# Optimization experiments

Hardware: AMD Instinct MI355X
Metric: run time of the kernel (lower is better)

The kernel has to match this reference:

```python
import jax, jax.numpy as jnp
import numpy as np

B = 1024          # batch
H = 1024          # rnn_num_hidden
T = 512           # max_length (encoder timesteps)
NUM = 44          # numeric features
EMB = [(30490, 64), (7, 8), (12, 8), (3, 4)]
IN = NUM + sum(d for _, d in EMB)   # input_size = 128


def lstm_cell(x, h, c, w_ih, w_hh, b_ih, b_hh):
    # PyTorch LSTM gate order: i, f, g, o
    g = x @ w_ih.T + h @ w_hh.T + b_ih + b_hh
    i, f, gg, o = jnp.split(g, 4, axis=-1)
    c2 = jax.nn.sigmoid(f) * c + jax.nn.sigmoid(i) * jnp.tanh(gg)
    h2 = jax.nn.sigmoid(o) * jnp.tanh(c2)
    return h2, c2


def setup_inputs():
    key = jax.random.key(0)
    ks = iter(jax.random.split(key, 32))
    nrm = lambda shape, s=0.02: (s * jax.random.normal(next(ks), shape)).astype(jnp.float32)
    return {
        "x": nrm((B, 1, NUM), 1.0),
        "x_emb": jax.random.randint(next(ks), (B, 1, 4), 0, 3),
        "h0": nrm((2, B, H), 1.0),
        "c0": nrm((2, B, H), 1.0),
        "encoder_outputs": nrm((T, B, H), 1.0),
        "emb0": nrm(EMB[0]), "emb1": nrm(EMB[1]), "emb2": nrm(EMB[2]), "emb3": nrm(EMB[3]),
        "attn_w": nrm((T, IN + 2 * H)), "attn_b": nrm((T,)),
        "comb_w": nrm((IN, IN + H)), "comb_b": nrm((IN,)),
        "w_ih0": nrm((4 * H, IN)), "w_hh0": nrm((4 * H, H)),
        "b_ih0": nrm((4 * H,)), "b_hh0": nrm((4 * H,)),
        "w_ih1": nrm((4 * H, H)), "w_hh1": nrm((4 * H, H)),
        "b_ih1": nrm((4 * H,)), "b_hh1": nrm((4 * H,)),
        "pred_w": nrm((1, H)), "pred_b": nrm((1,)),
    }


def reference(x, x_emb, h0, c0, encoder_outputs, emb0, emb1, emb2, emb3,
              attn_w, attn_b, comb_w, comb_b,
              w_ih0, w_hh0, b_ih0, b_hh0, w_ih1, w_hh1, b_ih1, b_hh1,
              pred_w, pred_b):
    xt = x.transpose(1, 0, 2)[0]                       # (B, NUM)
    ids = x_emb.transpose(1, 0, 2)[0]                  # (B, 4)
    e = jnp.concatenate([emb0[ids[:, 0]], emb1[ids[:, 1]],
                         emb2[ids[:, 2]], emb3[ids[:, 3]]], axis=1)
    x_rnn = jnp.concatenate([xt, e], axis=1)           # (B, IN)
    attn_in = jnp.concatenate([x_rnn, h0[0], c0[0]], axis=1)       # (B, IN+2H)
    aw = jax.nn.softmax(attn_in @ attn_w.T + attn_b, axis=1)       # (B, T)
    ctx = jnp.einsum('bt,tbh->bh', aw, encoder_outputs)            # (B, H)
    comb = jnp.concatenate([x_rnn, ctx], axis=1) @ comb_w.T + comb_b  # (B, IN)
    h1, c1 = lstm_cell(comb, h0[0], c0[0], w_ih0, w_hh0, b_ih0, b_hh0)
    h2, c2 = lstm_cell(h1, h0[1], c0[1], w_ih1, w_hh1, b_ih1, b_hh1)
    out = h2 @ pred_w.T + pred_b                       # (B, 1)
    return out, (jnp.stack([h1, h2]), jnp.stack([c1, c2])), aw
```

## Files before the change

kernel.cpp:

```cpp
#include <hip/hip_runtime.h>
#include <hip/hip_bf16.h>

#define B 1024
#define H 1024
#define T 512
#define NUM 44
#define IN 128
#define AK (IN + 2 * H)
#define XC (IN + H)
#define G4 (4 * H)
#define BH ((size_t)B * H)

typedef __attribute__((ext_vector_type(8))) short s16x8;
typedef __attribute__((ext_vector_type(4))) float f32x4;

__device__ __forceinline__ unsigned short f2bf(float f) {
    unsigned u = __float_as_uint(f);
    unsigned r = (u + 0x7fffu + ((u >> 16) & 1u)) >> 16;
    return (unsigned short)r;
}
__device__ __forceinline__ float bf2f(unsigned short u) {
    return __uint_as_float(((unsigned)u) << 16);
}
__device__ __forceinline__ float sigmf(float v) { return 1.0f / (1.0f + expf(-v)); }

__device__ __forceinline__ void gload16(const ushort* g, ushort* l) {
    __builtin_amdgcn_global_load_lds(
        (const __attribute__((address_space(1))) void*)g,
        (__attribute__((address_space(3))) void*)l,
        16, 0, 0);
}

#define TM 128
#define TN 128
#define TK 32

__device__ __forceinline__ void gemm_core(
    const ushort* __restrict__ X, const ushort* __restrict__ W,
    float* __restrict__ Cf, ushort* __restrict__ Cb,
    int kbeg, int kend, int ldx, int ldw, int ldc,
    int m0, int n0, ushort (*As)[TK], ushort (*Bs)[TK])
{
    const int tid = threadIdx.x;
    const int lane = tid & 63;
    const int wid = tid >> 6;
    const int wm = wid >> 1, wn = wid & 1;
    const int srow = wid * 32 + (lane >> 2);
    const int skc  = (lane & 3) * 8;

    f32x4 acc[4][4] = {};

    for (int k0 = kbeg; k0 < kend; k0 += TK) {
        gload16(X + (size_t)(m0 + srow) * ldx + k0 + skc,      &As[wid * 32][0]);
        gload16(X + (size_t)(m0 + srow + 16) * ldx + k0 + skc, &As[wid * 32 + 16][0]);
        gload16(W + (size_t)(n0 + srow) * ldw + k0 + skc,      &Bs[wid * 32][0]);
        gload16(W + (size_t)(n0 + srow + 16) * ldw + k0 + skc, &Bs[wid * 32 + 16][0]);
        __syncthreads();

        s16x8 a[4], b[4];
        #pragma unroll
        for (int m = 0; m < 4; ++m)
            a[m] = *(const s16x8*)&As[wm * 64 + m * 16 + (lane & 15)][(lane >> 4) * 8];
        #pragma unroll
        for (int n = 0; n < 4; ++n)
            b[n] = *(const s16x8*)&Bs[wn * 64 + n * 16 + (lane & 15)][(lane >> 4) * 8];
        #pragma unroll
        for (int m = 0; m < 4; ++m)
            #pragma unroll
            for (int n = 0; n < 4; ++n)
                acc[m][n] = __builtin_amdgcn_mfma_f32_16x16x32_bf16(a[m], b[n], acc[m][n], 0, 0, 0);
        __syncthreads();
    }

    #pragma unroll
    for (int m = 0; m < 4; ++m) {
        #pragma unroll
        for (int n = 0; n < 4; ++n) {
            int col = n0 + wn * 64 + n * 16 + (lane & 15);
            #pragma unroll
            for (int j = 0; j < 4; ++j) {
                int row = m0 + wm * 64 + m * 16 + (lane >> 4) * 4 + j;
                float v = acc[m][n][j];
                if (Cf) Cf[(size_t)row * ldc + col] = v;
                if (Cb) Cb[(size_t)row * ldc + col] = f2bf(v);
            }
        }
    }
}

__global__ __launch_bounds__(256) void allgemms_kernel(
    const ushort* __restrict__ attn_in, const ushort* __restrict__ attn_w_bf,
    float* __restrict__ logits_p,
    const ushort* __restrict__ h0_bf,
    const ushort* __restrict__ whh0_bf, const ushort* __restrict__ whh1_bf,
    ushort* __restrict__ g1part, ushort* __restrict__ g2part,
    const ushort* __restrict__ wih0_bf, const ushort* __restrict__ comb_wT_bf,
    ushort* __restrict__ W_f_bf)
{
    __shared__ ushort As[TM][TK];
    __shared__ ushort Bs[TN][TK];
    const int rid = blockIdx.x;
    if (rid < 128) {
        int z = rid >> 5, t = rid & 31;
        int m0 = (t >> 2) * TM, n0 = (t & 3) * TN;
        gemm_core(attn_in, attn_w_bf, logits_p + (size_t)z * B * T, nullptr,
                  z * 544, z * 544 + 544, AK, AK, T, m0, n0, As, Bs);
    } else if (rid < 640) {
        int layer = (rid - 128) >> 8;
        int t = (rid - 128) & 255;
        int m0 = (t >> 5) * TM, n0 = (t & 31) * TN;
        gemm_core(h0_bf + (size_t)layer * BH, layer ? whh1_bf : whh0_bf,
                  nullptr, layer ? g2part : g1part,
                  0, H, H, H, G4, m0, n0, As, Bs);
    } else {
        int t = rid - 640;
        int m0 = (t / 9) * TM, n0 = (t % 9) * TN;
        gemm_core(wih0_bf, comb_wT_bf, nullptr, W_f_bf,
                  0, IN, IN, IN, XC, m0, n0, As, Bs);
    }
}

__global__ __launch_bounds__(256) void gemm64_kernel(
    const ushort* __restrict__ X, const ushort* __restrict__ W,
    const float* __restrict__ bias1, const float* __restrict__ bias2,
    const ushort* __restrict__ CinBf, ushort* __restrict__ Cb,
    int K, int ldx, int ldw, int ldc)
{
    __shared__ ushort As[64][TK];
    __shared__ ushort Bs[128][TK];
    const int tid = threadIdx.x;
    const int lane = tid & 63;
    const int wid = tid >> 6;
    const int wm = wid >> 1, wn = wid & 1;
    const int m0 = blockIdx.y * 64;
    const int n0 = blockIdx.x * 128;
    const int skc = (lane & 3) * 8;

    f32x4 acc[2][4] = {};

    for (int k0 = 0; k0 < K; k0 += TK) {
        gload16(X + (size_t)(m0 + wid * 16 + (lane >> 2)) * ldx + k0 + skc, &As[wid * 16][0]);
        gload16(W + (size_t)(n0 + wid * 32 + (lane >> 2)) * ldw + k0 + skc, &Bs[wid * 32][0]);
        gload16(W + (size_t)(n0 + wid * 32 + 16 + (lane >> 2)) * ldw + k0 + skc, &Bs[wid * 32 + 16][0]);
        __syncthreads();
        s16x8 a[2], b[4];
        #pragma unroll
        for (int m = 0; m < 2; ++m)
            a[m] = *(const s16x8*)&As[wm * 32 + m * 16 + (lane & 15)][(lane >> 4) * 8];
        #pragma unroll
        for (int n = 0; n < 4; ++n)
            b[n] = *(const s16x8*)&Bs[wn * 64 + n * 16 + (lane & 15)][(lane >> 4) * 8];
        #pragma unroll
        for (int m = 0; m < 2; ++m)
            #pragma unroll
            for (int n = 0; n < 4; ++n)
                acc[m][n] = __builtin_amdgcn_mfma_f32_16x16x32_bf16(a[m], b[n], acc[m][n], 0, 0, 0);
        __syncthreads();
    }

    #pragma unroll
    for (int m = 0; m < 2; ++m) {
        #pragma unroll
        for (int n = 0; n < 4; ++n) {
            int col = n0 + wn * 64 + n * 16 + (lane & 15);
            float badd = (bias1 ? bias1[col] : 0.f) + (bias2 ? bias2[col] : 0.f);
            #pragma unroll
            for (int j = 0; j < 4; ++j) {
                int row = m0 + wm * 32 + m * 16 + (lane >> 4) * 4 + j;
                float v = acc[m][n][j] + badd + bf2f(CinBf[(size_t)row * ldc + col]);
                Cb[(size_t)row * ldc + col] = f2bf(v);
            }
        }
    }
}

#define P0 2048
#define P1 (P0 + 1088)
#define P2 (P1 + 512)
#define P3 (P2 + 4096)
#define P4 (P3 + 4096)
#define P5 (P4 + 4096)
#define P6 (P5 + 576)
#define P7 (P6 + 16)
#define P8 (P7 + 1024)

__global__ __launch_bounds__(256) void preamble_kernel(
    const float* __restrict__ h0, const float* __restrict__ attn_w,
    const float* __restrict__ w_ih0, const float* __restrict__ w_hh0,
    const float* __restrict__ w_ih1, const float* __restrict__ w_hh1,
    const float* __restrict__ comb_w, const float* __restrict__ comb_b,
    const float* __restrict__ b_ih0, const float* __restrict__ b_hh0,
    const float* __restrict__ x, const int* __restrict__ x_emb,
    const float* __restrict__ c0,
    const float* __restrict__ e0, const float* __restrict__ e1,
    const float* __restrict__ e2, const float* __restrict__ e3,
    ushort* __restrict__ h0_bf, ushort* __restrict__ attn_w_bf,
    ushort* __restrict__ wih0_bf, ushort* __restrict__ whh0_bf,
    ushort* __restrict__ wih1_bf, ushort* __restrict__ whh1_bf,
    ushort* __restrict__ comb_wT, float* __restrict__ biasf,
    ushort* __restrict__ attn_in, ushort* __restrict__ xctx)
{
    const int bid = blockIdx.x;
    const int tid = threadIdx.x;

    if (bid < P5) {
        const float* s; ushort* d; int f;
        if (bid < P0)      { f = bid * 256 + tid;        s = h0;     d = h0_bf; }
        else if (bid < P1) { f = (bid - P0) * 256 + tid; s = attn_w; d = attn_w_bf; }
        else if (bid < P2) { f = (bid - P1) * 256 + tid; s = w_ih0;  d = wih0_bf; }
        else if (bid < P3) { f = (bid - P2) * 256 + tid; s = w_hh0;  d = whh0_bf; }
        else if (bid < P4) { f = (bid - P3) * 256 + tid; s = w_ih1;  d = wih1_bf; }
        else               { f = (bid - P4) * 256 + tid; s = w_hh1;  d = whh1_bf; }
        float4 v = ((const float4*)s)[f];
        ushort4 o = {f2bf(v.x), f2bf(v.y), f2bf(v.z), f2bf(v.w)};
        ((ushort4*)d)[f] = o;
    } else if (bid < P6) {
        int e = (bid - P5) * 256 + tid;
        int j = e >> 7, k = e & 127;
        comb_wT[e] = f2bf(comb_w[(size_t)k * XC + j]);
    } else if (bid < P7) {
        __shared__ float cb[IN];
        for (int i = tid; i < IN; i += 256) cb[i] = comb_b[i];
        __syncthreads();
        int i = (bid - P6) * 256 + tid;
        float s = b_ih0[i] + b_hh0[i];
        const float* row = w_ih0 + (size_t)i * IN;
        #pragma unroll 8
        for (int j = 0; j < IN; ++j) s += row[j] * cb[j];
        biasf[i] = s;
    } else {
        int b = bid - P7;
        int id0 = x_emb[b * 4 + 0];
        int id1 = x_emb[b * 4 + 1];
        int id2 = x_emb[b * 4 + 2];
        int id3 = x_emb[b * 4 + 3];
        ushort* dst = attn_in + (size_t)b * AK;
        for (int j = tid; j < AK; j += 256) {
            float v;
            if (j < 44)        v = x[b * NUM + j];
            else if (j < 108)  v = e0[id0 * 64 + (j - 44)];
            else if (j < 116)  v = e1[id1 * 8 + (j - 108)];
            else if (j < 124)  v = e2[id2 * 8 + (j - 116)];
            else if (j < 128)  v = e3[id3 * 4 + (j - 124)];
            else if (j < 1152) v = h0[b * H + (j - 128)];
            else               v = c0[b * H + (j - 1152)];
            unsigned short bf = f2bf(v);
            dst[j] = bf;
            if (j < IN) xctx[(size_t)b * XC + j] = bf;
        }
    }
}

__global__ __launch_bounds__(256) void softmax_kernel(
    const float* __restrict__ logits_p, const float* __restrict__ attn_b,
    float* __restrict__ aw)
{
    int b = blockIdx.x;
    int tid = threadIdx.x;
    __shared__ float red[8];
    float v0 = attn_b[tid], v1 = attn_b[tid + 256];
    #pragma unroll
    for (int z = 0; z < 4; ++z) {
        const float* lp = logits_p + (size_t)z * B * T + (size_t)b * T;
        v0 += lp[tid];
        v1 += lp[tid + 256];
    }
    float m = fmaxf(v0, v1);
    #pragma unroll
    for (int off = 32; off > 0; off >>= 1) m = fmaxf(m, __shfl_down(m, off, 64));
    if ((tid & 63) == 0) red[tid >> 6] = m;
    __syncthreads();
    m = fmaxf(fmaxf(red[0], red[1]), fmaxf(red[2], red[3]));
    float e0 = expf(v0 - m), e1 = expf(v1 - m);
    float s = e0 + e1;
    #pragma unroll
    for (int off = 32; off > 0; off >>= 1) s += __shfl_down(s, off, 64);
    if ((tid & 63) == 0) red[4 + (tid >> 6)] = s;
    __syncthreads();
    s = red[4] + red[5] + red[6] + red[7];
    float inv = 1.0f / s;
    aw[(size_t)b * T + tid]       = e0 * inv;
    aw[(size_t)b * T + tid + 256] = e1 * inv;
}

__global__ __launch_bounds__(256) void ctx_kernel(
    const float* __restrict__ enc, const float* __restrict__ aw,
    float* __restrict__ ctxp)
{
    const int b = blockIdx.x >> 1;
    const int z = blockIdx.x & 1;
    const int tid = threadIdx.x;
    __shared__ float w[256];
    w[tid] = aw[(size_t)b * T + z * 256 + tid];
    __syncthreads();

    const float* p = enc + (size_t)(z * 256) * BH + (size_t)b * H + tid * 4;
    float4 acc = {0.f, 0.f, 0.f, 0.f};
    for (int t0 = 0; t0 < 256; t0 += 8) {
        float4 vv[8];
        #pragma unroll
        for (int u = 0; u < 8; ++u)
            vv[u] = *(const float4*)(p + (size_t)(t0 + u) * BH);
        #pragma unroll
        for (int u = 0; u < 8; ++u) {
            float sw = w[t0 + u];
            acc.x += sw * vv[u].x; acc.y += sw * vv[u].y;
            acc.z += sw * vv[u].z; acc.w += sw * vv[u].w;
        }
    }
    *(float4*)(ctxp + (size_t)z * BH + (size_t)b * H + tid * 4) = acc;
}

__global__ __launch_bounds__(256) void ctx_reduce_kernel(
    const float* __restrict__ ctxp, ushort* __restrict__ xctx)
{
    int i = blockIdx.x * 256 + threadIdx.x;
    float4 a = ((const float4*)ctxp)[i];
    float4 c = ((const float4*)(ctxp + BH))[i];
    int f = i * 4;
    int b = f >> 10, h = f & 1023;
    ushort4 o = {f2bf(a.x + c.x), f2bf(a.y + c.y), f2bf(a.z + c.z), f2bf(a.w + c.w)};
    *(ushort4*)(xctx + (size_t)b * XC + IN + h) = o;
}

__global__ __launch_bounds__(256) void lstm_pointwise_kernel(
    const ushort* __restrict__ g, const float* __restrict__ c_in,
    float* __restrict__ h_out, float* __restrict__ c_out,
    ushort* __restrict__ h_bf)
{
    int q = blockIdx.x * 256 + threadIdx.x;
    int b = q >> 8;
    int j = (q & 255) * 4;
    const ushort* gr = g + (size_t)b * G4 + j;
    ushort4 gi4 = *(const ushort4*)(gr);
    ushort4 gf4 = *(const ushort4*)(gr + H);
    ushort4 gc4 = *(const ushort4*)(gr + 2 * H);
    ushort4 go4 = *(const ushort4*)(gr + 3 * H);
    size_t base = (size_t)b * H + j;
    float4 cin = *(const float4*)(c_in + base);
    float4 cv, hv;
    {
        float c0v = sigmf(bf2f(gf4.x)) * cin.x + sigmf(bf2f(gi4.x)) * tanhf(bf2f(gc4.x));
        float c1v = sigmf(bf2f(gf4.y)) * cin.y + sigmf(bf2f(gi4.y)) * tanhf(bf2f(gc4.y));
        float c2v = sigmf(bf2f(gf4.z)) * cin.z + sigmf(bf2f(gi4.z)) * tanhf(bf2f(gc4.z));
        float c3v = sigmf(bf2f(gf4.w)) * cin.w + sigmf(bf2f(gi4.w)) * tanhf(bf2f(gc4.w));
        cv = make_float4(c0v, c1v, c2v, c3v);
        hv = make_float4(sigmf(bf2f(go4.x)) * tanhf(c0v), sigmf(bf2f(go4.y)) * tanhf(c1v),
                         sigmf(bf2f(go4.z)) * tanhf(c2v), sigmf(bf2f(go4.w)) * tanhf(c3v));
    }
    *(float4*)(c_out + base) = cv;
    *(float4*)(h_out + base) = hv;
    if (h_bf) {
        ushort4 o = {f2bf(hv.x), f2bf(hv.y), f2bf(hv.z), f2bf(hv.w)};
        *(ushort4*)(h_bf + base) = o;
    }
}

__global__ __launch_bounds__(256) void pred_kernel(
    const float* __restrict__ h2, const float* __restrict__ pw,
    const float* __restrict__ pb, float* __restrict__ out)
{
    int b = blockIdx.x;
    const float* row = h2 + (size_t)b * H;
    float s = 0.f;
    for (int j = threadIdx.x; j < H; j += 256) s += row[j] * pw[j];
    #pragma unroll
    for (int off = 32; off > 0; off >>= 1) s += __shfl_down(s, off, 64);
    __shared__ float sm[4];
    if ((threadIdx.x & 63) == 0) sm[threadIdx.x >> 6] = s;
    __syncthreads();
    if (threadIdx.x == 0) out[b] = sm[0] + sm[1] + sm[2] + sm[3] + pb[0];
}

extern "C" void kernel_launch(void* const* d_in, const int* in_sizes, int n_in,
                              void* d_out, int out_size, void* d_ws, size_t ws_size,
                              hipStream_t stream) {
    (void)in_sizes; (void)n_in; (void)out_size; (void)ws_size;
    const float* x      = (const float*)d_in[0];
    const int*   x_emb  = (const int*)d_in[1];
    const float* h0     = (const float*)d_in[2];
    const float* c0     = (const float*)d_in[3];
    const float* enc    = (const float*)d_in[4];
    const float* emb0   = (const float*)d_in[5];
    const float* emb1   = (const float*)d_in[6];
    const float* emb2   = (const float*)d_in[7];
    const float* emb3   = (const float*)d_in[8];
    const float* attn_w = (const float*)d_in[9];
    const float* attn_b = (const float*)d_in[10];
    const float* comb_w = (const float*)d_in[11];
    const float* comb_b = (const float*)d_in[12];
    const float* w_ih0  = (const float*)d_in[13];
    const float* w_hh0  = (const float*)d_in[14];
    const float* b_ih0  = (const float*)d_in[15];
    const float* b_hh0  = (const float*)d_in[16];
    const float* w_ih1  = (const float*)d_in[17];
    const float* w_hh1  = (const float*)d_in[18];
    const float* b_ih1  = (const float*)d_in[19];
    const float* b_hh1  = (const float*)d_in[20];
    const float* pred_w = (const float*)d_in[21];
    const float* pred_b = (const float*)d_in[22];

    float* out = (float*)d_out;
    float* h1_out = out + 1024;
    float* h2_out = out + 1024 + BH;
    float* c1_out = out + 1024 + 2 * BH;
    float* c2_out = out + 1024 + 3 * BH;
    float* aw_out = out + 1024 + 4 * BH;

    char* w = (char*)d_ws;
    ushort* attn_in_bf = (ushort*)w;  w += (size_t)B * AK * 2;
    ushort* h0_bf      = (ushort*)w;  w += (size_t)2 * BH * 2;
    ushort* attn_w_bf  = (ushort*)w;  w += (size_t)T * AK * 2;
    ushort* wih0_bf    = (ushort*)w;  w += (size_t)G4 * IN * 2;
    ushort* whh0_bf    = (ushort*)w;  w += (size_t)G4 * H * 2;
    ushort* wih1_bf    = (ushort*)w;  w += (size_t)G4 * H * 2;
    ushort* whh1_bf    = (ushort*)w;  w += (size_t)G4 * H * 2;
    ushort* comb_wT_bf = (ushort*)w;  w += (size_t)XC * IN * 2;
    ushort* W_f_bf     = (ushort*)w;  w += (size_t)G4 * XC * 2;
    float*  bias_f     = (float*)w;   w += (size_t)G4 * 4;
    ushort* xctx_bf    = (ushort*)w;  w += (size_t)B * XC * 2;
    ushort* h1_bf      = (ushort*)w;  w += (size_t)BH * 2;
    ushort* g1part     = (ushort*)w;  w += (size_t)B * G4 * 2;
    ushort* g2part     = (ushort*)w;  w += (size_t)B * G4 * 2;
    float*  logits_p   = (float*)w;   w += (size_t)4 * B * T * 4;
    float*  ctxp       = (float*)w;   w += (size_t)2 * BH * 4;

    preamble_kernel<<<P8, 256, 0, stream>>>(
        h0, attn_w, w_ih0, w_hh0, w_ih1, w_hh1, comb_w, comb_b, b_ih0, b_hh0,
        x, x_emb, c0, emb0, emb1, emb2, emb3,
        h0_bf, attn_w_bf, wih0_bf, whh0_bf, wih1_bf, whh1_bf, comb_wT_bf, bias_f,
        attn_in_bf, xctx_bf);

    allgemms_kernel<<<928, 256, 0, stream>>>(
        attn_in_bf, attn_w_bf, logits_p,
        h0_bf, whh0_bf, whh1_bf, g1part, g2part,
        wih0_bf, comb_wT_bf, W_f_bf);

    softmax_kernel<<<B, 256, 0, stream>>>(logits_p, attn_b, aw_out);

    ctx_kernel<<<2048, 256, 0, stream>>>(enc, aw_out, ctxp);

    ctx_reduce_kernel<<<(int)(BH / 4 / 256), 256, 0, stream>>>(ctxp, xctx_bf);

    gemm64_kernel<<<dim3(G4 / 128, B / 64), 256, 0, stream>>>(
        xctx_bf, W_f_bf, bias_f, nullptr, g1part, g1part, XC, XC, XC, G4);

    lstm_pointwise_kernel<<<(int)(BH / 4 / 256), 256, 0, stream>>>(g1part, c0, h1_out, c1_out, h1_bf);

    gemm64_kernel<<<dim3(G4 / 128, B / 64), 256, 0, stream>>>(
        h1_bf, wih1_bf, b_ih1, b_hh1, g2part, g2part, H, H, H, G4);

    lstm_pointwise_kernel<<<(int)(BH / 4 / 256), 256, 0, stream>>>(g2part, c0 + BH, h2_out, c2_out, nullptr);

    pred_kernel<<<B, 256, 0, stream>>>(h2_out, pred_w, pred_b, out);
}
```

Measured before the change: 590.6 us.

## Interleave LSTM gate rows and fuse pointwise cell into the input GEMM epilogue

Weight rows of all LSTM matrices and the biases are permuted during preamble conversion so that the four gates of each hidden unit sit in adjacent output columns. The second-stage GEMM epilogue then gathers the i/f/g/o pre-activations with lane shuffles and computes c and h directly, which removes both standalone pointwise kernels and the bf16 round-trip of the full gate buffer. Only one lane in four writes, so epilogue stores become scattered and less coalesced, and the transcendentals are computed redundantly in all four lanes.

```diff
diff --git a/kernel.cpp b/kernel.cpp
--- a/kernel.cpp
+++ b/kernel.cpp
@@ -92,9 +92,9 @@
     const ushort* __restrict__ attn_in, const ushort* __restrict__ attn_w_bf,
     float* __restrict__ logits_p,
     const ushort* __restrict__ h0_bf,
-    const ushort* __restrict__ whh0_bf, const ushort* __restrict__ whh1_bf,
+    const ushort* __restrict__ whh0p, const ushort* __restrict__ whh1p,
     ushort* __restrict__ g1part, ushort* __restrict__ g2part,
-    const ushort* __restrict__ wih0_bf, const ushort* __restrict__ comb_wT_bf,
+    const ushort* __restrict__ wih0p, const ushort* __restrict__ comb_wT_bf,
     ushort* __restrict__ W_f_bf)
 {
     __shared__ ushort As[TM][TK];
@@ -109,22 +109,22 @@
         int layer = (rid - 128) >> 8;
         int t = (rid - 128) & 255;
         int m0 = (t >> 5) * TM, n0 = (t & 31) * TN;
-        gemm_core(h0_bf + (size_t)layer * BH, layer ? whh1_bf : whh0_bf,
+        gemm_core(h0_bf + (size_t)layer * BH, layer ? whh1p : whh0p,
                   nullptr, layer ? g2part : g1part,
                   0, H, H, H, G4, m0, n0, As, Bs);
     } else {
         int t = rid - 640;
         int m0 = (t / 9) * TM, n0 = (t % 9) * TN;
-        gemm_core(wih0_bf, comb_wT_bf, nullptr, W_f_bf,
+        gemm_core(wih0p, comb_wT_bf, nullptr, W_f_bf,
                   0, IN, IN, IN, XC, m0, n0, As, Bs);
     }
 }
 
-__global__ __launch_bounds__(256) void gemm64_kernel(
+__global__ __launch_bounds__(256) void gemm64_lstm_kernel(
     const ushort* __restrict__ X, const ushort* __restrict__ W,
-    const float* __restrict__ bias1, const float* __restrict__ bias2,
-    const ushort* __restrict__ CinBf, ushort* __restrict__ Cb,
-    int K, int ldx, int ldw, int ldc)
+    const float* __restrict__ biasp, const ushort* __restrict__ CinBf,
+    const float* __restrict__ c_in, float* __restrict__ h_out, float* __restrict__ c_out,
+    ushort* __restrict__ h_bf, int K)
 {
     __shared__ ushort As[64][TK];
     __shared__ ushort Bs[128][TK];
@@ -139,9 +139,9 @@
     f32x4 acc[2][4] = {};
 
     for (int k0 = 0; k0 < K; k0 += TK) {
-        gload16(X + (size_t)(m0 + wid * 16 + (lane >> 2)) * ldx + k0 + skc, &As[wid * 16][0]);
-        gload16(W + (size_t)(n0 + wid * 32 + (lane >> 2)) * ldw + k0 + skc, &Bs[wid * 32][0]);
-        gload16(W + (size_t)(n0 + wid * 32 + 16 + (lane >> 2)) * ldw + k0 + skc, &Bs[wid * 32 + 16][0]);
+        gload16(X + (size_t)(m0 + wid * 16 + (lane >> 2)) * K + k0 + skc, &As[wid * 16][0]);
+        gload16(W + (size_t)(n0 + wid * 32 + (lane >> 2)) * K + k0 + skc, &Bs[wid * 32][0]);
+        gload16(W + (size_t)(n0 + wid * 32 + 16 + (lane >> 2)) * K + k0 + skc, &Bs[wid * 32 + 16][0]);
         __syncthreads();
         s16x8 a[2], b[4];
         #pragma unroll
@@ -158,17 +158,33 @@
         __syncthreads();
     }
 
+    const int q = lane & 3;
     #pragma unroll
     for (int m = 0; m < 2; ++m) {
         #pragma unroll
         for (int n = 0; n < 4; ++n) {
             int col = n0 + wn * 64 + n * 16 + (lane & 15);
-            float badd = (bias1 ? bias1[col] : 0.f) + (bias2 ? bias2[col] : 0.f);
+            int u = col >> 2;
+            float badd = biasp[col];
             #pragma unroll
             for (int j = 0; j < 4; ++j) {
                 int row = m0 + wm * 32 + m * 16 + (lane >> 4) * 4 + j;
-                float v = acc[m][n][j] + badd + bf2f(CinBf[(size_t)row * ldc + col]);
-                Cb[(size_t)row * ldc + col] = f2bf(v);
+                float pre = acc[m][n][j] + badd + bf2f(CinBf[(size_t)row * G4 + col]);
+                float f1 = __shfl_xor(pre, 1, 64);
+                float f2 = __shfl_xor(pre, 2, 64);
+                float f3 = __shfl_xor(pre, 3, 64);
+                float gi = q == 0 ? pre : q == 1 ? f1 : q == 2 ? f2 : f3;
+                float gf = q == 0 ? f1 : q == 1 ? pre : q == 2 ? f3 : f2;
+                float gg = q == 0 ? f2 : q == 1 ? f3 : q == 2 ? pre : f1;
+                float go = q == 0 ? f3 : q == 1 ? f2 : q == 2 ? f1 : pre;
+                float cprev = c_in[(size_t)row * H + u];
+                float c = sigmf(gf) * cprev + sigmf(gi) * tanhf(gg);
+                float h = sigmf(go) * tanhf(c);
+                if (q == 0) {
+                    h_out[(size_t)row * H + u] = h;
+                    c_out[(size_t)row * H + u] = c;
+                    if (h_bf) h_bf[(size_t)row * H + u] = f2bf(h);
+                }
             }
         }
     }
@@ -182,7 +198,8 @@
 #define P5 (P4 + 4096)
 #define P6 (P5 + 576)
 #define P7 (P6 + 16)
-#define P8 (P7 + 1024)
+#define P8 (P7 + 16)
+#define P9 (P8 + 1024)
 
 __global__ __launch_bounds__(256) void preamble_kernel(
     const float* __restrict__ h0, const float* __restrict__ attn_w,
@@ -190,28 +207,42 @@
     const float* __restrict__ w_ih1, const float* __restrict__ w_hh1,
     const float* __restrict__ comb_w, const float* __restrict__ comb_b,
     const float* __restrict__ b_ih0, const float* __restrict__ b_hh0,
+    const float* __restrict__ b_ih1, const float* __restrict__ b_hh1,
     const float* __restrict__ x, const int* __restrict__ x_emb,
     const float* __restrict__ c0,
     const float* __restrict__ e0, const float* __restrict__ e1,
     const float* __restrict__ e2, const float* __restrict__ e3,
     ushort* __restrict__ h0_bf, ushort* __restrict__ attn_w_bf,
-    ushort* __restrict__ wih0_bf, ushort* __restrict__ whh0_bf,
-    ushort* __restrict__ wih1_bf, ushort* __restrict__ whh1_bf,
-    ushort* __restrict__ comb_wT, float* __restrict__ biasf,
+    ushort* __restrict__ wih0p, ushort* __restrict__ whh0p,
+    ushort* __restrict__ wih1p, ushort* __restrict__ whh1p,
+    ushort* __restrict__ comb_wT, float* __restrict__ biasf, float* __restrict__ bias2p,
     ushort* __restrict__ attn_in, ushort* __restrict__ xctx)
 {
     const int bid = blockIdx.x;
     const int tid = threadIdx.x;
 
-    if (bid < P5) {
+    if (bid < P1) {
         const float* s; ushort* d; int f;
-        if (bid < P0)      { f = bid * 256 + tid;        s = h0;     d = h0_bf; }
-        else if (bid < P1) { f = (bid - P0) * 256 + tid; s = attn_w; d = attn_w_bf; }
-        else if (bid < P2) { f = (bid - P1) * 256 + tid; s = w_ih0;  d = wih0_bf; }
-        else if (bid < P3) { f = (bid - P2) * 256 + tid; s = w_hh0;  d = whh0_bf; }
-        else if (bid < P4) { f = (bid - P3) * 256 + tid; s = w_ih1;  d = wih1_bf; }
-        else               { f = (bid - P4) * 256 + tid; s = w_hh1;  d = whh1_bf; }
+        if (bid < P0) { f = bid * 256 + tid;        s = h0;     d = h0_bf; }
+        else          { f = (bid - P0) * 256 + tid; s = attn_w; d = attn_w_bf; }
         float4 v = ((const float4*)s)[f];
+        ushort4 o = {f2bf(v.x), f2bf(v.y), f2bf(v.z), f2bf(v.w)};
+        ((ushort4*)d)[f] = o;
+    } else if (bid < P2) {
+        int f = (bid - P1) * 256 + tid;
+        int r = f >> 5, c = f & 31;
+        int srcrow = ((r & 3) << 10) + (r >> 2);
+        float4 v = ((const float4*)w_ih0)[srcrow * 32 + c];
+        ushort4 o = {f2bf(v.x), f2bf(v.y), f2bf(v.z), f2bf(v.w)};
+        ((ushort4*)wih0p)[f] = o;
+    } else if (bid < P5) {
+        const float* s; ushort* d; int f;
+        if (bid < P3)      { f = (bid - P2) * 256 + tid; s = w_hh0; d = whh0p; }
+        else if (bid < P4) { f = (bid - P3) * 256 + tid; s = w_ih1; d = wih1p; }
+        else               { f = (bid - P4) * 256 + tid; s = w_hh1; d = whh1p; }
+        int r = f >> 8, c = f & 255;
+        int srcrow = ((r & 3) << 10) + (r >> 2);
+        float4 v = ((const float4*)s)[srcrow * 256 + c];
         ushort4 o = {f2bf(v.x), f2bf(v.y), f2bf(v.z), f2bf(v.w)};
         ((ushort4*)d)[f] = o;
     } else if (bid < P6) {
@@ -222,14 +253,19 @@
         __shared__ float cb[IN];
         for (int i = tid; i < IN; i += 256) cb[i] = comb_b[i];
         __syncthreads();
-        int i = (bid - P6) * 256 + tid;
-        float s = b_ih0[i] + b_hh0[i];
-        const float* row = w_ih0 + (size_t)i * IN;
+        int p = (bid - P6) * 256 + tid;
+        int srow = ((p & 3) << 10) + (p >> 2);
+        float s = b_ih0[srow] + b_hh0[srow];
+        const float* row = w_ih0 + (size_t)srow * IN;
         #pragma unroll 8
         for (int j = 0; j < IN; ++j) s += row[j] * cb[j];
-        biasf[i] = s;
+        biasf[p] = s;
+    } else if (bid < P8) {
+        int p = (bid - P7) * 256 + tid;
+        int srow = ((p & 3) << 10) + (p >> 2);
+        bias2p[p] = b_ih1[srow] + b_hh1[srow];
     } else {
-        int b = bid - P7;
+        int b = bid - P8;
         int id0 = x_emb[b * 4 + 0];
         int id1 = x_emb[b * 4 + 1];
         int id2 = x_emb[b * 4 + 2];
@@ -321,39 +357,6 @@
     int b = f >> 10, h = f & 1023;
     ushort4 o = {f2bf(a.x + c.x), f2bf(a.y + c.y), f2bf(a.z + c.z), f2bf(a.w + c.w)};
     *(ushort4*)(xctx + (size_t)b * XC + IN + h) = o;
-}
-
-__global__ __launch_bounds__(256) void lstm_pointwise_kernel(
-    const ushort* __restrict__ g, const float* __restrict__ c_in,
-    float* __restrict__ h_out, float* __restrict__ c_out,
-    ushort* __restrict__ h_bf)
-{
-    int q = blockIdx.x * 256 + threadIdx.x;
-    int b = q >> 8;
-    int j = (q & 255) * 4;
-    const ushort* gr = g + (size_t)b * G4 + j;
-    ushort4 gi4 = *(const ushort4*)(gr);
-    ushort4 gf4 = *(const ushort4*)(gr + H);
-    ushort4 gc4 = *(const ushort4*)(gr + 2 * H);
-    ushort4 go4 = *(const ushort4*)(gr + 3 * H);
-    size_t base = (size_t)b * H + j;
-    float4 cin = *(const float4*)(c_in + base);
-    float4 cv, hv;
-    {
-        float c0v = sigmf(bf2f(gf4.x)) * cin.x + sigmf(bf2f(gi4.x)) * tanhf(bf2f(gc4.x));
-        float c1v = sigmf(bf2f(gf4.y)) * cin.y + sigmf(bf2f(gi4.y)) * tanhf(bf2f(gc4.y));
-        float c2v = sigmf(bf2f(gf4.z)) * cin.z + sigmf(bf2f(gi4.z)) * tanhf(bf2f(gc4.z));
-        float c3v = sigmf(bf2f(gf4.w)) * cin.w + sigmf(bf2f(gi4.w)) * tanhf(bf2f(gc4.w));
-        cv = make_float4(c0v, c1v, c2v, c3v);
-        hv = make_float4(sigmf(bf2f(go4.x)) * tanhf(c0v), sigmf(bf2f(go4.y)) * tanhf(c1v),
-                         sigmf(bf2f(go4.z)) * tanhf(c2v), sigmf(bf2f(go4.w)) * tanhf(c3v));
-    }
-    *(float4*)(c_out + base) = cv;
-    *(float4*)(h_out + base) = hv;
-    if (h_bf) {
-        ushort4 o = {f2bf(hv.x), f2bf(hv.y), f2bf(hv.z), f2bf(hv.w)};
-        *(ushort4*)(h_bf + base) = o;
-    }
 }
 
 __global__ __launch_bounds__(256) void pred_kernel(
@@ -411,13 +414,14 @@
     ushort* attn_in_bf = (ushort*)w;  w += (size_t)B * AK * 2;
     ushort* h0_bf      = (ushort*)w;  w += (size_t)2 * BH * 2;
     ushort* attn_w_bf  = (ushort*)w;  w += (size_t)T * AK * 2;
-    ushort* wih0_bf    = (ushort*)w;  w += (size_t)G4 * IN * 2;
-    ushort* whh0_bf    = (ushort*)w;  w += (size_t)G4 * H * 2;
-    ushort* wih1_bf    = (ushort*)w;  w += (size_t)G4 * H * 2;
-    ushort* whh1_bf    = (ushort*)w;  w += (size_t)G4 * H * 2;
+    ushort* wih0p      = (ushort*)w;  w += (size_t)G4 * IN * 2;
+    ushort* whh0p      = (ushort*)w;  w += (size_t)G4 * H * 2;
+    ushort* wih1p      = (ushort*)w;  w += (size_t)G4 * H * 2;
+    ushort* whh1p      = (ushort*)w;  w += (size_t)G4 * H * 2;
     ushort* comb_wT_bf = (ushort*)w;  w += (size_t)XC * IN * 2;
     ushort* W_f_bf     = (ushort*)w;  w += (size_t)G4 * XC * 2;
     float*  bias_f     = (float*)w;   w += (size_t)G4 * 4;
+    float*  bias2p     = (float*)w;   w += (size_t)G4 * 4;
     ushort* xctx_bf    = (ushort*)w;  w += (size_t)B * XC * 2;
     ushort* h1_bf      = (ushort*)w;  w += (size_t)BH * 2;
     ushort* g1part     = (ushort*)w;  w += (size_t)B * G4 * 2;
@@ -425,16 +429,17 @@
     float*  logits_p   = (float*)w;   w += (size_t)4 * B * T * 4;
     float*  ctxp       = (float*)w;   w += (size_t)2 * BH * 4;
 
-    preamble_kernel<<<P8, 256, 0, stream>>>(
-        h0, attn_w, w_ih0, w_hh0, w_ih1, w_hh1, comb_w, comb_b, b_ih0, b_hh0,
+    preamble_kernel<<<P9, 256, 0, stream>>>(
+        h0, attn_w, w_ih0, w_hh0, w_ih1, w_hh1, comb_w, comb_b,
+        b_ih0, b_hh0, b_ih1, b_hh1,
         x, x_emb, c0, emb0, emb1, emb2, emb3,
-        h0_bf, attn_w_bf, wih0_bf, whh0_bf, wih1_bf, whh1_bf, comb_wT_bf, bias_f,
-        attn_in_bf, xctx_bf);
+        h0_bf, attn_w_bf, wih0p, whh0p, wih1p, whh1p, comb_wT_bf,
+        bias_f, bias2p, attn_in_bf, xctx_bf);
 
     allgemms_kernel<<<928, 256, 0, stream>>>(
         attn_in_bf, attn_w_bf, logits_p,
-        h0_bf, whh0_bf, whh1_bf, g1part, g2part,
-        wih0_bf, comb_wT_bf, W_f_bf);
+        h0_bf, whh0p, whh1p, g1part, g2part,
+        wih0p, comb_wT_bf, W_f_bf);
 
     softmax_kernel<<<B, 256, 0, stream>>>(logits_p, attn_b, aw_out);
 
@@ -442,15 +447,11 @@
 
     ctx_reduce_kernel<<<(int)(BH / 4 / 256), 256, 0, stream>>>(ctxp, xctx_bf);
 
-    gemm64_kernel<<<dim3(G4 / 128, B / 64), 256, 0, stream>>>(
-        xctx_bf, W_f_bf, bias_f, nullptr, g1part, g1part, XC, XC, XC, G4);
-
-    lstm_pointwise_kernel<<<(int)(BH / 4 / 256), 256, 0, stream>>>(g1part, c0, h1_out, c1_out, h1_bf);
-
-    gemm64_kernel<<<dim3(G4 / 128, B / 64), 256, 0, stream>>>(
-        h1_bf, wih1_bf, b_ih1, b_hh1, g2part, g2part, H, H, H, G4);
-
-    lstm_pointwise_kernel<<<(int)(BH / 4 / 256), 256, 0, stream>>>(g2part, c0 + BH, h2_out, c2_out, nullptr);
+    gemm64_lstm_kernel<<<dim3(G4 / 128, B / 64), 256, 0, stream>>>(
+        xctx_bf, W_f_bf, bias_f, g1part, c0, h1_out, c1_out, h1_bf, XC);
+
+    gemm64_lstm_kernel<<<dim3(G4 / 128, B / 64), 256, 0, stream>>>(
+        h1_bf, wih1p, bias2p, g2part, c0 + BH, h2_out, c2_out, nullptr, H);
 
     pred_kernel<<<B, 256, 0, stream>>>(h2_out, pred_w, pred_b, out);
 }
```

Result: slower. 618.9 us (+4.8%).
